# Kernel tuning notes

Hardware: AMD Instinct MI355X
Metric: run time of the kernel (lower is better)

The kernel has to match this reference:

```python
import jax, jax.numpy as jnp
import numpy as np

PATCH_LEN = 16


def _forward(x, W_proj, b_proj, W_router, b_router, W_experts, b_experts, W_head, b_head):
    # x: (B, L, C); Model drops first 2 channels
    seq_len = x.shape[1]
    xs = x[:, :, 2:]                                   # (B, L, N)
    B, L, N = xs.shape
    # CI=True: 'b l n -> (b n) l 1' (track as (BN, L) since trailing dim is 1)
    ci = jnp.transpose(xs, (0, 2, 1)).reshape(B * N, L)
    # RevIN-style instance norm (means detached in torch)
    means = jax.lax.stop_gradient(jnp.mean(ci, axis=1, keepdims=True))
    xc = ci - means
    stdev = jnp.sqrt(jnp.var(xc, axis=1, keepdims=True) + 1e-5)  # unbiased=False
    xc = xc / stdev
    # non-overlapping patching: unfold(1, pl, pl)
    p = L // PATCH_LEN
    patches = xc[:, : p * PATCH_LEN].reshape(B * N, p, PATCH_LEN)
    xp = patches @ W_proj.T + b_proj                   # (BN, p, d)
    gates = jax.nn.softmax(xp @ W_router.T + b_router, axis=-1)  # (BN, p, E)
    # soft-routed mixture of linear experts: sum_e gate_e * (xp @ W_e^T + b_e)
    eo = jnp.einsum('tpd,ehd->tpeh', xp, W_experts) + b_experts  # (BN, p, E, d)
    combined = jnp.einsum('tpeh,tpe->tph', eo, gates)            # (BN, p, d)
    d = combined.shape[-1]
    flat = combined.reshape(B * N, p * d)              # '(b n) p d -> b (p d) n', n=1
    if p * d < seq_len:
        flat = jnp.pad(flat, ((0, 0), (0, seq_len - p * d)))
    else:
        flat = flat[:, :seq_len]
    flat = flat * stdev + means                        # de-normalize (BN, L)
    # '(b n) l 1 -> b l n' then 'b l n -> b n l' == reshape to (B, N, L)
    temporal = flat.reshape(B, N, seq_len)
    out = temporal @ W_head.T + b_head                 # linear_head: (B, N, pred)
    out = jnp.transpose(out, (0, 2, 1))[:, :, :1]      # 'b n d -> b d n', keep var 0
    return out


def setup_inputs() -> dict:
    key = jax.random.key(0)
    ks = jax.random.split(key, 12)
    B, L, C = 32, 1024, 34
    d, E, pl, pred = 256, 8, PATCH_LEN, 96
    return {
        'x': jax.random.normal(ks[0], (B, L, C), dtype=jnp.float32),
        'x_mark_enc': jax.random.normal(ks[1], (B, L, 4), dtype=jnp.float32),
        'x_dec': jax.random.normal(ks[2], (B, pred, C), dtype=jnp.float32),
        'x_mark_dec': jax.random.normal(ks[3], (B, pred, 4), dtype=jnp.float32),
        'W_proj': jax.random.normal(ks[4], (d, pl), dtype=jnp.float32) * 0.1,
        'b_proj': jax.random.normal(ks[5], (d,), dtype=jnp.float32) * 0.02,
        'W_router': jax.random.normal(ks[6], (E, d), dtype=jnp.float32) * 0.05,
        'b_router': jax.random.normal(ks[7], (E,), dtype=jnp.float32) * 0.02,
        'W_experts': jax.random.normal(ks[8], (E, d, d), dtype=jnp.float32) * 0.05,
        'b_experts': jax.random.normal(ks[9], (E, d), dtype=jnp.float32) * 0.02,
        'W_head': jax.random.normal(ks[10], (pred, L), dtype=jnp.float32) * 0.03,
        'b_head': jax.random.normal(ks[11], (pred,), dtype=jnp.float32) * 0.02,
    }


def reference(x, x_mark_enc, x_dec, x_mark_dec, W_proj, b_proj, W_router, b_router,
              W_experts, b_experts, W_head, b_head):
    # x_mark_enc, x_dec, x_mark_dec are accepted but unused by Model.forward
    return _forward(x, W_proj, b_proj, W_router, b_router,
                    W_experts, b_experts, W_head, b_head)
```

## Files before the change

### kernel.cpp

```cpp
#include <hip/hip_runtime.h>
#include <math.h>


#define NB 32
#define LSEQ 1024
#define CCH 34
#define NP 4
#define DMODEL 256
#define NEXP 8
#define PRED 96

#define WT_FLOATS    (NEXP * DMODEL * DMODEL)
#define XP_FLOATS    (NB * NP * DMODEL)
#define GATES_FLOATS (NB * NP * NEXP)
#define STATS_FLOATS (NB * 2)
#define FLAT_FLOATS  (NEXP * NB * LSEQ)

__global__ __launch_bounds__(256) void k_stats(
    const float* __restrict__ x,
    const float* __restrict__ W_proj, const float* __restrict__ b_proj,
    const float* __restrict__ W_router, const float* __restrict__ b_router,
    const float* __restrict__ W_experts, float* __restrict__ Wt,
    float* __restrict__ xp_ws, float* __restrict__ gates_ws,
    float* __restrict__ stats_ws)
{
    const int b = blockIdx.x;
    const int tid = threadIdx.x;

    __shared__ float tile[64][33];
    __shared__ float xn[LSEQ];
    __shared__ float xp_s[NP * DMODEL];
    __shared__ float red[8];
    __shared__ float lg[32];
    __shared__ float mean_s, rstd_s;

    float v[4];
    #pragma unroll
    for (int i = 0; i < 4; ++i)
        v[i] = x[(size_t)(b * LSEQ + tid + 256 * i) * CCH + 2];

    {
        const int e  = b >> 2;
        const int h0 = (b & 3) * 64;
        const float* src = W_experts + ((size_t)e << 16);
        float*       dst = Wt        + ((size_t)e << 16);
        const int dx  = tid & 31, hy = tid >> 5;
        const int hx  = tid & 63, dy = tid >> 6;
        for (int d0 = 0; d0 < DMODEL; d0 += 32) {
            #pragma unroll
            for (int i = 0; i < 8; ++i) {
                const int hh = hy + 8 * i;
                tile[hh][dx] = src[(size_t)(h0 + hh) * DMODEL + d0 + dx];
            }
            __syncthreads();
            #pragma unroll
            for (int i = 0; i < 8; ++i) {
                const int dd = dy + 4 * i;
                dst[(size_t)(d0 + dd) * DMODEL + h0 + hx] = tile[hx][dd];
            }
            __syncthreads();
        }
    }

    float s = 0.f, sq = 0.f;
    #pragma unroll
    for (int i = 0; i < 4; ++i) { s += v[i]; sq += v[i] * v[i]; }
    #pragma unroll
    for (int off = 32; off > 0; off >>= 1) {
        s  += __shfl_down(s,  off);
        sq += __shfl_down(sq, off);
    }
    const int wave = tid >> 6;
    if ((tid & 63) == 0) { red[wave * 2] = s; red[wave * 2 + 1] = sq; }
    __syncthreads();
    if (tid == 0) {
        const float S = red[0] + red[2] + red[4] + red[6];
        const float Q = red[1] + red[3] + red[5] + red[7];
        const float mean = S * (1.0f / LSEQ);
        const float var  = Q * (1.0f / LSEQ) - mean * mean;
        const float stdv = sqrtf(var + 1e-5f);
        mean_s = mean;
        rstd_s = 1.0f / stdv;
        stats_ws[b * 2]     = mean;
        stats_ws[b * 2 + 1] = stdv;
    }
    __syncthreads();
    const float mean = mean_s, rstd = rstd_s;
    #pragma unroll
    for (int i = 0; i < 4; ++i)
        xn[tid + 256 * i] = (v[i] - mean) * rstd;
    __syncthreads();

    {
        const int h = tid;
        float wrow[16];
        #pragma unroll
        for (int j = 0; j < 16; ++j) wrow[j] = W_proj[h * 16 + j];
        const float bp = b_proj[h];
        #pragma unroll
        for (int p = 0; p < NP; ++p) {
            float acc = bp;
            #pragma unroll
            for (int j = 0; j < 16; ++j) acc += xn[p * 16 + j] * wrow[j];
            xp_s[p * DMODEL + h] = acc;
            xp_ws[((size_t)b * NP + p) * DMODEL + h] = acc;
        }
    }
    __syncthreads();

    if (tid < 32) {
        const int p = tid >> 3, e = tid & 7;
        float acc = b_router[e];
        const float* wr = W_router + e * DMODEL;
        const float* xp = xp_s + p * DMODEL;
        #pragma unroll 8
        for (int h = 0; h < DMODEL; ++h) acc += xp[h] * wr[h];
        lg[tid] = acc;
    }
    __syncthreads();

    if (tid < NP) {
        const int p = tid;
        float m = -1e30f;
        #pragma unroll
        for (int e = 0; e < NEXP; ++e) m = fmaxf(m, lg[p * 8 + e]);
        float ex[NEXP];
        float sum = 0.f;
        #pragma unroll
        for (int e = 0; e < NEXP; ++e) { ex[e] = expf(lg[p * 8 + e] - m); sum += ex[e]; }
        const float inv = 1.0f / sum;
        #pragma unroll
        for (int e = 0; e < NEXP; ++e)
            gates_ws[((size_t)b * NP + p) * NEXP + e] = ex[e] * inv;
    }
}

__global__ __launch_bounds__(256) void k_expert(
    const float* __restrict__ Wt, const float* __restrict__ b_experts,
    const float* __restrict__ xp_ws, const float* __restrict__ gates_ws,
    float* __restrict__ flat_part)
{
    const int bid = blockIdx.x;
    const int b  = bid >> 5;
    const int r  = bid & 31;
    const int hq = r >> 3;
    const int e  = r & 7;
    const int tid = threadIdx.x;
    const int p  = tid >> 6;
    const int hl = tid & 63;
    const int h  = (hq << 6) + hl;

    __shared__ float xp_s[NP * DMODEL];
    __shared__ float g_s[NP * NEXP];

    #pragma unroll
    for (int i = 0; i < 4; ++i)
        xp_s[tid + 256 * i] = xp_ws[(size_t)b * (NP * DMODEL) + tid + 256 * i];
    if (tid < NP * NEXP) g_s[tid] = gates_ws[(size_t)b * (NP * NEXP) + tid];
    __syncthreads();

    const float* xp = xp_s + (p << 8);
    const float* wt = Wt + ((size_t)e << 16) + h;
    const float bias = b_experts[(e << 8) + h];
    const float gate = g_s[(p << 3) + e];

    float d0 = 0.f, d1 = 0.f, d2 = 0.f, d3 = 0.f;
    #pragma unroll 4
    for (int d = 0; d < DMODEL; d += 4) {
        d0 += wt[(size_t)(d + 0) << 8] * xp[d + 0];
        d1 += wt[(size_t)(d + 1) << 8] * xp[d + 1];
        d2 += wt[(size_t)(d + 2) << 8] * xp[d + 2];
        d3 += wt[(size_t)(d + 3) << 8] * xp[d + 3];
    }
    const float dot = (d0 + d1) + (d2 + d3);
    flat_part[(((size_t)e * NB + b) << 10) + (p << 8) + h] = gate * (dot + bias);
}

__global__ __launch_bounds__(256) void k_expert_direct(
    const float* __restrict__ W, const float* __restrict__ b_experts,
    const float* __restrict__ xp_ws, const float* __restrict__ gates_ws,
    float* __restrict__ flat_part)
{
    const int bid = blockIdx.x;
    const int b  = bid >> 5;
    const int r  = bid & 31;
    const int hq = r >> 3;
    const int e  = r & 7;
    const int tid = threadIdx.x;
    const int p  = tid >> 6;
    const int hl = tid & 63;
    const int h  = (hq << 6) + hl;

    __shared__ float xp_s[NP * DMODEL];
    __shared__ float g_s[NP * NEXP];

    #pragma unroll
    for (int i = 0; i < 4; ++i)
        xp_s[tid + 256 * i] = xp_ws[(size_t)b * (NP * DMODEL) + tid + 256 * i];
    if (tid < NP * NEXP) g_s[tid] = gates_ws[(size_t)b * (NP * NEXP) + tid];
    __syncthreads();

    const float4* xp4 = (const float4*)(xp_s + (p << 8));
    const float4* wrow = (const float4*)(W + (((size_t)e << 8) + h) * DMODEL);
    const float bias = b_experts[(e << 8) + h];
    const float gate = g_s[(p << 3) + e];

    float d0 = 0.f, d1 = 0.f, d2 = 0.f, d3 = 0.f;
    #pragma unroll 4
    for (int d = 0; d < DMODEL / 4; d += 4) {
        float4 w0 = wrow[d + 0], x0 = xp4[d + 0];
        float4 w1 = wrow[d + 1], x1 = xp4[d + 1];
        float4 w2 = wrow[d + 2], x2 = xp4[d + 2];
        float4 w3 = wrow[d + 3], x3 = xp4[d + 3];
        d0 += w0.x * x0.x + w0.y * x0.y + w0.z * x0.z + w0.w * x0.w;
        d1 += w1.x * x1.x + w1.y * x1.y + w1.z * x1.z + w1.w * x1.w;
        d2 += w2.x * x2.x + w2.y * x2.y + w2.z * x2.z + w2.w * x2.w;
        d3 += w3.x * x3.x + w3.y * x3.y + w3.z * x3.z + w3.w * x3.w;
    }
    const float dot = (d0 + d1) + (d2 + d3);
    flat_part[(((size_t)e * NB + b) << 10) + (p << 8) + h] = gate * (dot + bias);
}

__global__ __launch_bounds__(128) void k_head(
    const float* __restrict__ flat_part, const float* __restrict__ stats_ws,
    const float* __restrict__ W_head, const float* __restrict__ b_head,
    float* __restrict__ out)
{
    const int b = blockIdx.x;
    const int tid = threadIdx.x;
    __shared__ float f_s[LSEQ];

    const float mean = stats_ws[b * 2];
    const float stdv = stats_ws[b * 2 + 1];

    float4* f4s = (float4*)f_s;
    #pragma unroll
    for (int i = 0; i < 2; ++i) {
        const int idx = tid + 128 * i;
        float4 acc = make_float4(0.f, 0.f, 0.f, 0.f);
        #pragma unroll
        for (int e = 0; e < NEXP; ++e) {
            const float4 t = ((const float4*)(flat_part + (((size_t)e * NB + b) << 10)))[idx];
            acc.x += t.x; acc.y += t.y; acc.z += t.z; acc.w += t.w;
        }
        acc.x = acc.x * stdv + mean;
        acc.y = acc.y * stdv + mean;
        acc.z = acc.z * stdv + mean;
        acc.w = acc.w * stdv + mean;
        f4s[idx] = acc;
    }
    __syncthreads();

    if (tid < PRED) {
        const float4* wr = (const float4*)(W_head + (size_t)tid * LSEQ);
        const float4* f4 = (const float4*)f_s;
        float a0 = 0.f, a1 = 0.f, a2 = 0.f, a3 = 0.f;
        #pragma unroll 4
        for (int i = 0; i < LSEQ / 4; i += 4) {
            float4 w0 = wr[i + 0], x0 = f4[i + 0];
            float4 w1 = wr[i + 1], x1 = f4[i + 1];
            float4 w2 = wr[i + 2], x2 = f4[i + 2];
            float4 w3 = wr[i + 3], x3 = f4[i + 3];
            a0 += w0.x * x0.x + w0.y * x0.y + w0.z * x0.z + w0.w * x0.w;
            a1 += w1.x * x1.x + w1.y * x1.y + w1.z * x1.z + w1.w * x1.w;
            a2 += w2.x * x2.x + w2.y * x2.y + w2.z * x2.z + w2.w * x2.w;
            a3 += w3.x * x3.x + w3.y * x3.y + w3.z * x3.z + w3.w * x3.w;
        }
        out[(size_t)b * PRED + tid] = b_head[tid] + (a0 + a1) + (a2 + a3);
    }
}

extern "C" void kernel_launch(void* const* d_in, const int* in_sizes, int n_in,
                              void* d_out, int out_size, void* d_ws, size_t ws_size,
                              hipStream_t stream)
{
    const float* x         = (const float*)d_in[0];
    const float* W_proj    = (const float*)d_in[4];
    const float* b_proj    = (const float*)d_in[5];
    const float* W_router  = (const float*)d_in[6];
    const float* b_router  = (const float*)d_in[7];
    const float* W_experts = (const float*)d_in[8];
    const float* b_experts = (const float*)d_in[9];
    const float* W_head    = (const float*)d_in[10];
    const float* b_head    = (const float*)d_in[11];
    float* out = (float*)d_out;
    float* ws  = (float*)d_ws;

    const size_t need = (size_t)(WT_FLOATS + XP_FLOATS + GATES_FLOATS +
                                 STATS_FLOATS + FLAT_FLOATS);
    const bool use_t = ws_size >= need * sizeof(float);

    size_t off = use_t ? (size_t)WT_FLOATS : 0;
    float* Wt        = ws;
    float* xp_ws     = ws + off;  off += XP_FLOATS;
    float* gates_ws  = ws + off;  off += GATES_FLOATS;
    float* stats_ws  = ws + off;  off += STATS_FLOATS;
    float* flat_part = ws + off;

    if (use_t) {
        k_stats<<<NB, 256, 0, stream>>>(x, W_proj, b_proj, W_router, b_router,
                                        W_experts, Wt, xp_ws, gates_ws, stats_ws);
        k_expert<<<1024, 256, 0, stream>>>(Wt, b_experts, xp_ws, gates_ws, flat_part);
    } else {
        k_stats<<<NB, 256, 0, stream>>>(x, W_proj, b_proj, W_router, b_router,
                                        W_experts, ws, xp_ws, gates_ws, stats_ws);
        k_expert_direct<<<1024, 256, 0, stream>>>(W_experts, b_experts,
                                                  xp_ws, gates_ws, flat_part);
    }
    k_head<<<NB, 128, 0, stream>>>(flat_part, stats_ws, W_head, b_head, out);
}
```

Before: 118.2 us.

## Spread expert weight transpose over 256 blocks and parallelize head GEMV per wave

The W_experts transpose used to run as 8 serial tile steps inside each of 32 blocks. It is now split so each of 256 blocks transposes one 64x32 tile, and only the first 32 blocks go on to the stats, projection and routing work. The head kernel moves to 256 threads: each wave computes output rows by reading W_head coalesced across lanes and reducing with shuffles, replacing one thread per output walking a full row. This is meant to raise parallelism in the launch-bound stages, at the cost of more blocks in k_stats and extra shuffle reductions.

```diff
diff --git a/kernel.cpp b/kernel.cpp
--- a/kernel.cpp
+++ b/kernel.cpp
@@ -22,10 +22,11 @@
     const float* __restrict__ W_router, const float* __restrict__ b_router,
     const float* __restrict__ W_experts, float* __restrict__ Wt,
     float* __restrict__ xp_ws, float* __restrict__ gates_ws,
-    float* __restrict__ stats_ws)
-{
-    const int b = blockIdx.x;
+    float* __restrict__ stats_ws, int do_transpose)
+{
+    const int bid = blockIdx.x;
     const int tid = threadIdx.x;
+    const int b = bid;
 
     __shared__ float tile[64][33];
     __shared__ float xn[LSEQ];
@@ -35,32 +36,34 @@
     __shared__ float mean_s, rstd_s;
 
     float v[4];
-    #pragma unroll
-    for (int i = 0; i < 4; ++i)
-        v[i] = x[(size_t)(b * LSEQ + tid + 256 * i) * CCH + 2];
-
-    {
-        const int e  = b >> 2;
-        const int h0 = (b & 3) * 64;
+    if (b < NB) {
+        #pragma unroll
+        for (int i = 0; i < 4; ++i)
+            v[i] = x[(size_t)(b * LSEQ + tid + 256 * i) * CCH + 2];
+    }
+
+    if (do_transpose) {
+        const int e  = bid >> 5;
+        const int h0 = ((bid >> 3) & 3) << 6;
+        const int d0 = (bid & 7) << 5;
         const float* src = W_experts + ((size_t)e << 16);
         float*       dst = Wt        + ((size_t)e << 16);
-        const int dx  = tid & 31, hy = tid >> 5;
-        const int hx  = tid & 63, dy = tid >> 6;
-        for (int d0 = 0; d0 < DMODEL; d0 += 32) {
-            #pragma unroll
-            for (int i = 0; i < 8; ++i) {
-                const int hh = hy + 8 * i;
-                tile[hh][dx] = src[(size_t)(h0 + hh) * DMODEL + d0 + dx];
-            }
-            __syncthreads();
-            #pragma unroll
-            for (int i = 0; i < 8; ++i) {
-                const int dd = dy + 4 * i;
-                dst[(size_t)(d0 + dd) * DMODEL + h0 + hx] = tile[hx][dd];
-            }
-            __syncthreads();
-        }
-    }
+        const int dx = tid & 31, hy = tid >> 5;
+        const int hx = tid & 63, dy = tid >> 6;
+        #pragma unroll
+        for (int i = 0; i < 8; ++i) {
+            const int hh = hy + 8 * i;
+            tile[hh][dx] = src[(size_t)(h0 + hh) * DMODEL + d0 + dx];
+        }
+        __syncthreads();
+        #pragma unroll
+        for (int i = 0; i < 8; ++i) {
+            const int dd = dy + 4 * i;
+            dst[(size_t)(d0 + dd) * DMODEL + h0 + hx] = tile[hx][dd];
+        }
+    }
+
+    if (b >= NB) return;
 
     float s = 0.f, sq = 0.f;
     #pragma unroll
@@ -221,52 +224,55 @@
     flat_part[(((size_t)e * NB + b) << 10) + (p << 8) + h] = gate * (dot + bias);
 }
 
-__global__ __launch_bounds__(128) void k_head(
+__global__ __launch_bounds__(256) void k_head(
     const float* __restrict__ flat_part, const float* __restrict__ stats_ws,
     const float* __restrict__ W_head, const float* __restrict__ b_head,
     float* __restrict__ out)
 {
     const int b = blockIdx.x;
     const int tid = threadIdx.x;
-    __shared__ float f_s[LSEQ];
+    __shared__ float4 f4s[DMODEL];
 
     const float mean = stats_ws[b * 2];
     const float stdv = stats_ws[b * 2 + 1];
 
-    float4* f4s = (float4*)f_s;
-    #pragma unroll
-    for (int i = 0; i < 2; ++i) {
-        const int idx = tid + 128 * i;
+    {
         float4 acc = make_float4(0.f, 0.f, 0.f, 0.f);
         #pragma unroll
         for (int e = 0; e < NEXP; ++e) {
-            const float4 t = ((const float4*)(flat_part + (((size_t)e * NB + b) << 10)))[idx];
+            const float4 t = ((const float4*)(flat_part + (((size_t)e * NB + b) << 10)))[tid];
             acc.x += t.x; acc.y += t.y; acc.z += t.z; acc.w += t.w;
         }
         acc.x = acc.x * stdv + mean;
         acc.y = acc.y * stdv + mean;
         acc.z = acc.z * stdv + mean;
         acc.w = acc.w * stdv + mean;
-        f4s[idx] = acc;
-    }
-    __syncthreads();
-
-    if (tid < PRED) {
-        const float4* wr = (const float4*)(W_head + (size_t)tid * LSEQ);
-        const float4* f4 = (const float4*)f_s;
-        float a0 = 0.f, a1 = 0.f, a2 = 0.f, a3 = 0.f;
-        #pragma unroll 4
-        for (int i = 0; i < LSEQ / 4; i += 4) {
-            float4 w0 = wr[i + 0], x0 = f4[i + 0];
-            float4 w1 = wr[i + 1], x1 = f4[i + 1];
-            float4 w2 = wr[i + 2], x2 = f4[i + 2];
-            float4 w3 = wr[i + 3], x3 = f4[i + 3];
-            a0 += w0.x * x0.x + w0.y * x0.y + w0.z * x0.z + w0.w * x0.w;
-            a1 += w1.x * x1.x + w1.y * x1.y + w1.z * x1.z + w1.w * x1.w;
-            a2 += w2.x * x2.x + w2.y * x2.y + w2.z * x2.z + w2.w * x2.w;
-            a3 += w3.x * x3.x + w3.y * x3.y + w3.z * x3.z + w3.w * x3.w;
-        }
-        out[(size_t)b * PRED + tid] = b_head[tid] + (a0 + a1) + (a2 + a3);
+        f4s[tid] = acc;
+    }
+    __syncthreads();
+
+    const int lane = tid & 63;
+    const int w    = tid >> 6;
+
+    float4 fr[4];
+    #pragma unroll
+    for (int c = 0; c < 4; ++c) fr[c] = f4s[lane + 64 * c];
+
+    #pragma unroll 2
+    for (int i = 0; i < PRED / 4; ++i) {
+        const int k = w + 4 * i;
+        const float4* wr = (const float4*)(W_head + (size_t)k * LSEQ);
+        float a = 0.f;
+        #pragma unroll
+        for (int c = 0; c < 4; ++c) {
+            const float4 t = wr[lane + 64 * c];
+            a += t.x * fr[c].x + t.y * fr[c].y + t.z * fr[c].z + t.w * fr[c].w;
+        }
+        #pragma unroll
+        for (int off = 32; off > 0; off >>= 1)
+            a += __shfl_xor(a, off);
+        if (lane == 0)
+            out[(size_t)b * PRED + k] = b_head[k] + a;
     }
 }
 
@@ -297,15 +303,14 @@
     float* stats_ws  = ws + off;  off += STATS_FLOATS;
     float* flat_part = ws + off;
 
+    k_stats<<<256, 256, 0, stream>>>(x, W_proj, b_proj, W_router, b_router,
+                                     W_experts, Wt, xp_ws, gates_ws, stats_ws,
+                                     use_t ? 1 : 0);
     if (use_t) {
-        k_stats<<<NB, 256, 0, stream>>>(x, W_proj, b_proj, W_router, b_router,
-                                        W_experts, Wt, xp_ws, gates_ws, stats_ws);
         k_expert<<<1024, 256, 0, stream>>>(Wt, b_experts, xp_ws, gates_ws, flat_part);
     } else {
-        k_stats<<<NB, 256, 0, stream>>>(x, W_proj, b_proj, W_router, b_router,
-                                        W_experts, ws, xp_ws, gates_ws, stats_ws);
         k_expert_direct<<<1024, 256, 0, stream>>>(W_experts, b_experts,
                                                   xp_ws, gates_ws, flat_part);
     }
-    k_head<<<NB, 128, 0, stream>>>(flat_part, stats_ws, W_head, b_head, out);
-}
+    k_head<<<NB, 256, 0, stream>>>(flat_part, stats_ws, W_head, b_head, out);
+}
```

New measurement: 114.5 us. 3.1% less time.
